# Kernel optimization log

Hardware: AMD Instinct MI355X
Metric: run time of the kernel (lower is better)

Reference implementation:

```python
import jax, jax.numpy as jnp
import numpy as np

S_MIN, S_MAX, ALPHA = 1, 5, 5.0
EPS = 1e-6


def _conv2d_same(x, k):
    # x: [B,1,H,W], k: [1,1,3,3], stride 1, padding 1
    return jax.lax.conv_general_dilated(x, k, (1, 1), ((1, 1), (1, 1)),
                                        dimension_numbers=('NCHW', 'OIHW', 'NCHW'))


def sobel_complexity(x):
    # compute_spatial_complexity_sobel: per-image min-max normalized gradient magnitude
    xg = x.mean(1, keepdims=True)  # [B,1,H,W]
    sx = jnp.array([[1, 0, -1], [2, 0, -2], [1, 0, -1]], x.dtype).reshape(1, 1, 3, 3)
    sy = jnp.array([[1, 2, 1], [0, 0, 0], [-1, -2, -1]], x.dtype).reshape(1, 1, 3, 3)
    gx = _conv2d_same(xg, sx)
    gy = _conv2d_same(xg, sy)
    mag = jnp.sqrt(gx ** 2 + gy ** 2 + EPS)
    mn = mag.min((2, 3), keepdims=True)
    mx = mag.max((2, 3), keepdims=True)
    rng = mx - mn
    c = jnp.where(rng > 0, (mag - mn) / (rng + EPS), jnp.zeros_like(mag))
    return c[:, 0]  # [B,H,W]


def adaptive_steps(m):
    # adaptive_step_from_complexity, fully vectorized
    B, H, W = m.shape
    avg = jnp.ones((1, 1, 3, 3), m.dtype) / 9.0
    lc = _conv2d_same(m[:, None], avg)[:, 0]  # [B,H,W] local complexity
    hm, wm = H // 2, W // 2
    rc = jnp.stack([m[:, :hm, :wm].mean((1, 2)), m[:, :hm, wm:].mean((1, 2)),
                    m[:, hm:, :wm].mean((1, 2)), m[:, hm:, wm:].mean((1, 2))], axis=1)  # [B,4]
    base = S_MAX - jax.nn.sigmoid(ALPHA * (rc - 0.5)) * (S_MAX - S_MIN)
    base = jnp.round(jnp.clip(base, S_MIN, S_MAX)).astype(jnp.int32)  # [B,4]
    adj = jnp.round(jax.nn.sigmoid(ALPHA * (lc - 0.5)) * 2.0 - 1.0).astype(jnp.int32)  # [B,H,W]
    return jnp.clip(base[:, :, None, None] + adj[:, None], S_MIN, S_MAX)  # [B,4,H,W]


def _visits_lr(step):
    # step: [B,R,L] int. Left-to-right adaptive-step traversal along last axis per row.
    # Returns float mask [B,R,L] of visited positions.
    B, R, L = step.shape
    s = jnp.maximum(step, 1)

    def body(j, _):
        valid = j < L                       # [B,R]
        jc = jnp.minimum(j, L - 1)
        st = jnp.take_along_axis(s, jc[:, :, None], -1)[:, :, 0]
        return jnp.where(valid, j + st, j), (jc, valid)

    _, (jcs, valids) = jax.lax.scan(body, jnp.zeros((B, R), jnp.int32), None, length=L)
    jcs = jnp.moveaxis(jcs, 0, -1)          # [B,R,L]
    valids = jnp.moveaxis(valids, 0, -1)    # [B,R,L]
    bi = jnp.arange(B)[:, None, None]
    ri = jnp.arange(R)[None, :, None]
    vis = jnp.zeros((B, R, L), jnp.float32).at[bi, ri, jcs].add(valids.astype(jnp.float32))
    return (vis > 0).astype(jnp.float32)


def _visits_rl(step):
    # Right-to-left traversal == left-to-right on the mirrored step map, mirrored back.
    return jnp.flip(_visits_lr(jnp.flip(step, -1)), -1)


def _forward(x):
    m = sobel_complexity(x)                 # [B,H,W]
    steps = adaptive_steps(m)               # [B,4,H,W]
    v0 = _visits_lr(steps[:, 0])            # rows, left->right
    v1 = _visits_rl(steps[:, 1])            # rows, right->left
    v2 = jnp.swapaxes(_visits_lr(jnp.swapaxes(steps[:, 2], 1, 2)), 1, 2)  # cols, top->down
    v3 = jnp.swapaxes(_visits_rl(jnp.swapaxes(steps[:, 3], 1, 2)), 1, 2)  # cols, bottom->up
    V = v0 + v1 + v2 + v3                   # [B,H,W] visit counts
    # DirectionalScan followed by DirectionalMerge: output = sum_d x*visit_d / (V + 1e-6)
    return x * (V / (V + 1e-6))[:, None]


def setup_inputs() -> dict:
    key = jax.random.key(0)
    x = jax.random.normal(key, (8, 96, 256, 256), dtype=jnp.float32)
    return {"x": x}


def reference(x):
    return _forward(x)
```

## Files before the change

kernel.cpp:

```cpp
#include <hip/hip_runtime.h>
#include <math.h>

#define BB 8
#define CC 96
#define HH 256
#define WW 256
#define HW (HH*WW)

typedef unsigned long long u64;
typedef float f32x4 __attribute__((ext_vector_type(4)));

__global__ void k_mean(const float* __restrict__ x, float* __restrict__ m,
                       unsigned* __restrict__ mn_u, unsigned* __restrict__ mx_u) {
    if (blockIdx.x == 0 && threadIdx.x < 2 * BB) {
        if (threadIdx.x < BB) mn_u[threadIdx.x] = 0x7f800000u;
        else                  mx_u[threadIdx.x - BB] = 0u;
    }
    int blk = blockIdx.x;
    int b = blk >> 8, tile = blk & 255;
    int wv = threadIdx.x >> 6, ln = threadIdx.x & 63;
    int hw4 = tile * 64 + ln;
    const int per = HW / 4;
    const float4* xb = reinterpret_cast<const float4*>(x)
                     + ((size_t)b * CC + wv * 24) * per + hw4;
    double a0 = 0, a1 = 0, a2 = 0, a3 = 0;
#pragma unroll
    for (int c = 0; c < 24; ++c) {
        float4 v = xb[(size_t)c * per];
        a0 += (double)v.x; a1 += (double)v.y; a2 += (double)v.z; a3 += (double)v.w;
    }
    __shared__ double sbuf[4][4][64];
    sbuf[wv][0][ln] = a0; sbuf[wv][1][ln] = a1;
    sbuf[wv][2][ln] = a2; sbuf[wv][3][ln] = a3;
    __syncthreads();
    if (wv == 0) {
        double r0 = sbuf[0][0][ln] + sbuf[1][0][ln] + sbuf[2][0][ln] + sbuf[3][0][ln];
        double r1 = sbuf[0][1][ln] + sbuf[1][1][ln] + sbuf[2][1][ln] + sbuf[3][1][ln];
        double r2 = sbuf[0][2][ln] + sbuf[1][2][ln] + sbuf[2][2][ln] + sbuf[3][2][ln];
        double r3 = sbuf[0][3][ln] + sbuf[1][3][ln] + sbuf[2][3][ln] + sbuf[3][3][ln];
        float4 o;
        o.x = (float)(r0 / 96.0); o.y = (float)(r1 / 96.0);
        o.z = (float)(r2 / 96.0); o.w = (float)(r3 / 96.0);
        reinterpret_cast<float4*>(m)[(size_t)b * per + hw4] = o;
    }
}

__global__ void k_sobel(const float* __restrict__ m, float* __restrict__ mag,
                        unsigned* mn_u, unsigned* mx_u) {
    int row = blockIdx.x;
    int b = row >> 8, h = row & 255, w = threadIdx.x;
    const float* mb = m + (size_t)b * HW;
    auto at = [&](int hh, int ww) -> float {
        if (hh < 0 || hh >= HH || ww < 0 || ww >= WW) return 0.0f;
        return mb[hh * WW + ww];
    };
    float a00 = at(h - 1, w - 1), a01 = at(h - 1, w), a02 = at(h - 1, w + 1);
    float a10 = at(h, w - 1),                         a12 = at(h, w + 1);
    float a20 = at(h + 1, w - 1), a21 = at(h + 1, w), a22 = at(h + 1, w + 1);
    float gx = a00 - a02 + 2.0f * a10 - 2.0f * a12 + a20 - a22;
    float gy = a00 + 2.0f * a01 + a02 - a20 - 2.0f * a21 - a22;
    float mg = sqrtf(gx * gx + gy * gy + 1e-6f);
    mag[row * WW + w] = mg;

    float lmn = mg, lmx = mg;
    for (int off = 32; off; off >>= 1) {
        lmn = fminf(lmn, __shfl_down(lmn, off));
        lmx = fmaxf(lmx, __shfl_down(lmx, off));
    }
    __shared__ float smn[4], smx[4];
    int wv = threadIdx.x >> 6, ln = threadIdx.x & 63;
    if (ln == 0) { smn[wv] = lmn; smx[wv] = lmx; }
    __syncthreads();
    if (threadIdx.x == 0) {
        float bmn = fminf(fminf(smn[0], smn[1]), fminf(smn[2], smn[3]));
        float bmx = fmaxf(fmaxf(smx[0], smx[1]), fmaxf(smx[2], smx[3]));
        atomicMin(&mn_u[b], __float_as_uint(bmn));
        atomicMax(&mx_u[b], __float_as_uint(bmx));
    }
}

__global__ void k_adjpart(const float* __restrict__ mag, const unsigned* __restrict__ mn_u,
                          const unsigned* __restrict__ mx_u, signed char* __restrict__ adj,
                          float* __restrict__ part) {
    int row = blockIdx.x;
    int b = row >> 8, h = row & 255, w = threadIdx.x;
    float mn = __uint_as_float(mn_u[b]);
    float mx = __uint_as_float(mx_u[b]);
    float rng = mx - mn;
    const float* gb = mag + (size_t)b * HW;
    auto cat = [&](int hh, int ww) -> float {
        if (hh < 0 || hh >= HH || ww < 0 || ww >= WW) return 0.0f;
        float mg = gb[hh * WW + ww];
        return (rng > 0.0f) ? (mg - mn) / (rng + 1e-6f) : 0.0f;
    };
    float cc = cat(h, w);

    float r = cc;
    for (int off = 32; off; off >>= 1) r += __shfl_down(r, off);
    __shared__ float s[4];
    int wv = threadIdx.x >> 6, ln = threadIdx.x & 63;
    if (ln == 0) s[wv] = r;
    __syncthreads();
    if (threadIdx.x == 0) {
        part[row * 2 + 0] = s[0] + s[1];
        part[row * 2 + 1] = s[2] + s[3];
    }

    const float w9 = 1.0f / 9.0f;
    float acc = 0.0f;
    acc = fmaf(cat(h - 1, w - 1), w9, acc);
    acc = fmaf(cat(h - 1, w    ), w9, acc);
    acc = fmaf(cat(h - 1, w + 1), w9, acc);
    acc = fmaf(cat(h    , w - 1), w9, acc);
    acc = fmaf(cc,               w9, acc);
    acc = fmaf(cat(h    , w + 1), w9, acc);
    acc = fmaf(cat(h + 1, w - 1), w9, acc);
    acc = fmaf(cat(h + 1, w    ), w9, acc);
    acc = fmaf(cat(h + 1, w + 1), w9, acc);
    float sg = 1.0f / (1.0f + expf(-5.0f * (acc - 0.5f)));
    adj[row * WW + w] = (signed char)(int)rintf(sg * 2.0f - 1.0f);
}

#define SETBIT(j) do { int _j = (j); \
    if (_j < 64) m0 |= 1ull << _j; \
    else if (_j < 128) m1 |= 1ull << (_j - 64); \
    else if (_j < 192) m2 |= 1ull << (_j - 128); \
    else m3 |= 1ull << (_j - 192); } while (0)

__global__ void k_travbase(const signed char* __restrict__ adj, const float* __restrict__ part,
                           u64* __restrict__ masks) {
    int blk = blockIdx.x;
    int dir = blk >> 3, b = blk & 7;
    int t = threadIdx.x;

    __shared__ double sd[128];
    __shared__ int sbs;
    int hlo = (dir >> 1) ? 128 : 0;
    int col = dir & 1;
    if (t < 128) sd[t] = (double)part[((b << 8) + hlo + t) * 2 + col];
    __syncthreads();
    for (int str = 64; str > 0; str >>= 1) {
        if (t < str) sd[t] += sd[t + str];
        __syncthreads();
    }
    if (t == 0) {
        float rc = (float)(sd[0] / 16384.0);
        float sig = 1.0f / (1.0f + expf(-5.0f * (rc - 0.5f)));
        float bsf = 5.0f - sig * 4.0f;
        bsf = fminf(fmaxf(bsf, 1.0f), 5.0f);
        sbs = (int)rintf(bsf);
    }
    __syncthreads();
    int bs = sbs;

    int r = t;
    const signed char* ab = adj + (size_t)b * HW;
    u64 m0 = 0, m1 = 0, m2 = 0, m3 = 0;
    if (dir == 0) {
        int j = 0;
        while (j < WW) {
            SETBIT(j);
            int st = bs + (int)ab[r * WW + j];
            st = st < 1 ? 1 : (st > 5 ? 5 : st);
            j += st;
        }
    } else if (dir == 1) {
        int j = WW - 1;
        while (j >= 0) {
            SETBIT(j);
            int st = bs + (int)ab[r * WW + j];
            st = st < 1 ? 1 : (st > 5 ? 5 : st);
            j -= st;
        }
    } else if (dir == 2) {
        int j = 0;
        while (j < HH) {
            SETBIT(j);
            int st = bs + (int)ab[j * WW + r];
            st = st < 1 ? 1 : (st > 5 ? 5 : st);
            j += st;
        }
    } else {
        int j = HH - 1;
        while (j >= 0) {
            SETBIT(j);
            int st = bs + (int)ab[j * WW + r];
            st = st < 1 ? 1 : (st > 5 ? 5 : st);
            j -= st;
        }
    }
    u64* o = masks + ((size_t)dir * BB * 256 + (b << 8) + r) * 4;
    o[0] = m0; o[1] = m1; o[2] = m2; o[3] = m3;
}

__global__ void k_scale(const u64* __restrict__ masks, float* __restrict__ scale) {
    int row = blockIdx.x;
    int b = row >> 8, h = row & 255, w = threadIdx.x;
    const u64* m0 = masks + (((size_t)0 * BB + b) * 256 + h) * 4;
    const u64* m1 = masks + (((size_t)1 * BB + b) * 256 + h) * 4;
    const u64* m2 = masks + (((size_t)2 * BB + b) * 256 + w) * 4;
    const u64* m3 = masks + (((size_t)3 * BB + b) * 256 + w) * 4;
    int v = (int)((m0[w >> 6] >> (w & 63)) & 1ull)
          + (int)((m1[w >> 6] >> (w & 63)) & 1ull)
          + (int)((m2[h >> 6] >> (h & 63)) & 1ull)
          + (int)((m3[h >> 6] >> (h & 63)) & 1ull);
    float fV = (float)v;
    scale[row * WW + w] = fV / (fV + 1e-6f);
}

__global__ void k_out(const float* __restrict__ x, const float* __restrict__ scale,
                      float* __restrict__ out) {
    const int per_img4 = CC * HW / 4;
    const int hw4n = HW / 4;
    int i = blockIdx.x * blockDim.x + threadIdx.x;
    int b = i / per_img4;
    int hw4 = i & (hw4n - 1);
    f32x4 sv = reinterpret_cast<const f32x4*>(scale)[b * hw4n + hw4];
    f32x4 xv = reinterpret_cast<const f32x4*>(x)[i];
    f32x4 ov = xv * sv;
    __builtin_nontemporal_store(ov, reinterpret_cast<f32x4*>(out) + i);
}

extern "C" void kernel_launch(void* const* d_in, const int* in_sizes, int n_in,
                              void* d_out, int out_size, void* d_ws, size_t ws_size,
                              hipStream_t stream) {
    const float* x = (const float*)d_in[0];
    float* out = (float*)d_out;
    char* ws = (char*)d_ws;

    float* m     = (float*)(ws);
    float* mag   = (float*)(ws + (size_t)2 * 1024 * 1024);
    float* scale = (float*)(ws + (size_t)4 * 1024 * 1024);
    signed char* adj = (signed char*)(ws + (size_t)6 * 1024 * 1024);
    u64* masks   = (u64*)(ws + (size_t)6 * 1024 * 1024 + 524288);
    float* part  = (float*)(ws + (size_t)6 * 1024 * 1024 + 524288 + 262144);
    unsigned* mn_u = (unsigned*)(ws + (size_t)6 * 1024 * 1024 + 524288 + 262144 + 16384);
    unsigned* mx_u = mn_u + 8;

    k_mean<<<BB * 256, 256, 0, stream>>>(x, m, mn_u, mx_u);
    k_sobel<<<BB * HH, 256, 0, stream>>>(m, mag, mn_u, mx_u);
    k_adjpart<<<BB * HH, 256, 0, stream>>>(mag, mn_u, mx_u, adj, part);
    k_travbase<<<32, 256, 0, stream>>>(adj, part, masks);
    k_scale<<<BB * HH, 256, 0, stream>>>(masks, scale);
    k_out<<<(BB * CC * HW / 4) / 256, 256, 0, stream>>>(x, scale, out);
}
```

Measured before the change: 169.0 us.

## Fuse sobel, stencil, traversal and scale into one per-image kernel

Replaces four separate middle kernels with a single 1024-thread kernel per image. The per-image min/max comes from a block-level reduction, so the global atomics are gone, and the adj map and traversal masks now live in LDS instead of global memory. This is meant to cut launch overhead and global round-trips between the stages. In exchange the middle phase runs on only 8 blocks, each looping serially over 64K pixels several times, so latency and low parallelism may dominate.

```diff
diff --git a/kernel.cpp b/kernel.cpp
--- a/kernel.cpp
+++ b/kernel.cpp
@@ -10,12 +10,7 @@
 typedef unsigned long long u64;
 typedef float f32x4 __attribute__((ext_vector_type(4)));
 
-__global__ void k_mean(const float* __restrict__ x, float* __restrict__ m,
-                       unsigned* __restrict__ mn_u, unsigned* __restrict__ mx_u) {
-    if (blockIdx.x == 0 && threadIdx.x < 2 * BB) {
-        if (threadIdx.x < BB) mn_u[threadIdx.x] = 0x7f800000u;
-        else                  mx_u[threadIdx.x - BB] = 0u;
-    }
+__global__ void k_mean(const float* __restrict__ x, float* __restrict__ m) {
     int blk = blockIdx.x;
     int b = blk >> 8, tile = blk & 255;
     int wv = threadIdx.x >> 6, ln = threadIdx.x & 63;
@@ -45,167 +40,160 @@
     }
 }
 
-__global__ void k_sobel(const float* __restrict__ m, float* __restrict__ mag,
-                        unsigned* mn_u, unsigned* mx_u) {
-    int row = blockIdx.x;
-    int b = row >> 8, h = row & 255, w = threadIdx.x;
+#define SETBIT(j) do { int _j = (j); \
+    if (_j < 64) m0 |= 1ull << _j; \
+    else if (_j < 128) m1 |= 1ull << (_j - 64); \
+    else if (_j < 192) m2 |= 1ull << (_j - 128); \
+    else m3 |= 1ull << (_j - 192); } while (0)
+
+__global__ __launch_bounds__(1024)
+void k_middle(const float* __restrict__ m, float* __restrict__ mag,
+              float* __restrict__ scale) {
+    __shared__ signed char adj_s[HW];
+    __shared__ u64 mask_s[1024][4];
+    __shared__ float part_s[256][2];
+    __shared__ float partial_s[256][4];
+    __shared__ double sd[4][128];
+    __shared__ float red_mn[16], red_mx[16];
+    __shared__ float smn_f, smx_f;
+    __shared__ int sbs[4];
+
+    int b = blockIdx.x, tid = threadIdx.x;
     const float* mb = m + (size_t)b * HW;
+    float* gb = mag + (size_t)b * HW;
+    int wv = tid >> 6, ln = tid & 63;
+
     auto at = [&](int hh, int ww) -> float {
         if (hh < 0 || hh >= HH || ww < 0 || ww >= WW) return 0.0f;
         return mb[hh * WW + ww];
     };
-    float a00 = at(h - 1, w - 1), a01 = at(h - 1, w), a02 = at(h - 1, w + 1);
-    float a10 = at(h, w - 1),                         a12 = at(h, w + 1);
-    float a20 = at(h + 1, w - 1), a21 = at(h + 1, w), a22 = at(h + 1, w + 1);
-    float gx = a00 - a02 + 2.0f * a10 - 2.0f * a12 + a20 - a22;
-    float gy = a00 + 2.0f * a01 + a02 - a20 - 2.0f * a21 - a22;
-    float mg = sqrtf(gx * gx + gy * gy + 1e-6f);
-    mag[row * WW + w] = mg;
-
-    float lmn = mg, lmx = mg;
+
+    float lmn = __builtin_inff(), lmx = -__builtin_inff();
+    for (int p = 0; p < 64; ++p) {
+        int idx = p * 1024 + tid;
+        int h = idx >> 8, w = idx & 255;
+        float a00 = at(h - 1, w - 1), a01 = at(h - 1, w), a02 = at(h - 1, w + 1);
+        float a10 = at(h, w - 1),                         a12 = at(h, w + 1);
+        float a20 = at(h + 1, w - 1), a21 = at(h + 1, w), a22 = at(h + 1, w + 1);
+        float gx = a00 - a02 + 2.0f * a10 - 2.0f * a12 + a20 - a22;
+        float gy = a00 + 2.0f * a01 + a02 - a20 - 2.0f * a21 - a22;
+        float mg = sqrtf(gx * gx + gy * gy + 1e-6f);
+        gb[idx] = mg;
+        lmn = fminf(lmn, mg); lmx = fmaxf(lmx, mg);
+    }
     for (int off = 32; off; off >>= 1) {
         lmn = fminf(lmn, __shfl_down(lmn, off));
         lmx = fmaxf(lmx, __shfl_down(lmx, off));
     }
-    __shared__ float smn[4], smx[4];
-    int wv = threadIdx.x >> 6, ln = threadIdx.x & 63;
-    if (ln == 0) { smn[wv] = lmn; smx[wv] = lmx; }
-    __syncthreads();
-    if (threadIdx.x == 0) {
-        float bmn = fminf(fminf(smn[0], smn[1]), fminf(smn[2], smn[3]));
-        float bmx = fmaxf(fmaxf(smx[0], smx[1]), fmaxf(smx[2], smx[3]));
-        atomicMin(&mn_u[b], __float_as_uint(bmn));
-        atomicMax(&mx_u[b], __float_as_uint(bmx));
-    }
-}
-
-__global__ void k_adjpart(const float* __restrict__ mag, const unsigned* __restrict__ mn_u,
-                          const unsigned* __restrict__ mx_u, signed char* __restrict__ adj,
-                          float* __restrict__ part) {
-    int row = blockIdx.x;
-    int b = row >> 8, h = row & 255, w = threadIdx.x;
-    float mn = __uint_as_float(mn_u[b]);
-    float mx = __uint_as_float(mx_u[b]);
-    float rng = mx - mn;
-    const float* gb = mag + (size_t)b * HW;
+    if (ln == 0) { red_mn[wv] = lmn; red_mx[wv] = lmx; }
+    __syncthreads();
+    if (tid == 0) {
+        float a = red_mn[0], c2 = red_mx[0];
+        for (int i = 1; i < 16; ++i) { a = fminf(a, red_mn[i]); c2 = fmaxf(c2, red_mx[i]); }
+        smn_f = a; smx_f = c2;
+    }
+    __syncthreads();
+    float mn = smn_f, mx = smx_f, rng = mx - mn;
     auto cat = [&](int hh, int ww) -> float {
         if (hh < 0 || hh >= HH || ww < 0 || ww >= WW) return 0.0f;
         float mg = gb[hh * WW + ww];
         return (rng > 0.0f) ? (mg - mn) / (rng + 1e-6f) : 0.0f;
     };
-    float cc = cat(h, w);
-
-    float r = cc;
-    for (int off = 32; off; off >>= 1) r += __shfl_down(r, off);
-    __shared__ float s[4];
-    int wv = threadIdx.x >> 6, ln = threadIdx.x & 63;
-    if (ln == 0) s[wv] = r;
-    __syncthreads();
-    if (threadIdx.x == 0) {
-        part[row * 2 + 0] = s[0] + s[1];
-        part[row * 2 + 1] = s[2] + s[3];
-    }
-
+
+    int g = tid >> 8, w2 = tid & 255;
     const float w9 = 1.0f / 9.0f;
-    float acc = 0.0f;
-    acc = fmaf(cat(h - 1, w - 1), w9, acc);
-    acc = fmaf(cat(h - 1, w    ), w9, acc);
-    acc = fmaf(cat(h - 1, w + 1), w9, acc);
-    acc = fmaf(cat(h    , w - 1), w9, acc);
-    acc = fmaf(cc,               w9, acc);
-    acc = fmaf(cat(h    , w + 1), w9, acc);
-    acc = fmaf(cat(h + 1, w - 1), w9, acc);
-    acc = fmaf(cat(h + 1, w    ), w9, acc);
-    acc = fmaf(cat(h + 1, w + 1), w9, acc);
-    float sg = 1.0f / (1.0f + expf(-5.0f * (acc - 0.5f)));
-    adj[row * WW + w] = (signed char)(int)rintf(sg * 2.0f - 1.0f);
-}
-
-#define SETBIT(j) do { int _j = (j); \
-    if (_j < 64) m0 |= 1ull << _j; \
-    else if (_j < 128) m1 |= 1ull << (_j - 64); \
-    else if (_j < 192) m2 |= 1ull << (_j - 128); \
-    else m3 |= 1ull << (_j - 192); } while (0)
-
-__global__ void k_travbase(const signed char* __restrict__ adj, const float* __restrict__ part,
-                           u64* __restrict__ masks) {
-    int blk = blockIdx.x;
-    int dir = blk >> 3, b = blk & 7;
-    int t = threadIdx.x;
-
-    __shared__ double sd[128];
-    __shared__ int sbs;
-    int hlo = (dir >> 1) ? 128 : 0;
-    int col = dir & 1;
-    if (t < 128) sd[t] = (double)part[((b << 8) + hlo + t) * 2 + col];
+    for (int p = 0; p < 64; ++p) {
+        int h = p * 4 + g;
+        float cc = cat(h, w2);
+        float r = cc;
+        for (int off = 32; off; off >>= 1) r += __shfl_down(r, off);
+        if (ln == 0) partial_s[h][w2 >> 6] = r;
+        float acc = 0.0f;
+        acc = fmaf(cat(h - 1, w2 - 1), w9, acc);
+        acc = fmaf(cat(h - 1, w2    ), w9, acc);
+        acc = fmaf(cat(h - 1, w2 + 1), w9, acc);
+        acc = fmaf(cat(h    , w2 - 1), w9, acc);
+        acc = fmaf(cc,                w9, acc);
+        acc = fmaf(cat(h    , w2 + 1), w9, acc);
+        acc = fmaf(cat(h + 1, w2 - 1), w9, acc);
+        acc = fmaf(cat(h + 1, w2    ), w9, acc);
+        acc = fmaf(cat(h + 1, w2 + 1), w9, acc);
+        float sg = 1.0f / (1.0f + expf(-5.0f * (acc - 0.5f)));
+        adj_s[h * 256 + w2] = (signed char)(int)rintf(sg * 2.0f - 1.0f);
+    }
+    __syncthreads();
+    if (tid < 512) {
+        int row = tid >> 1, col = tid & 1;
+        part_s[row][col] = partial_s[row][2 * col] + partial_s[row][2 * col + 1];
+    }
+    __syncthreads();
+
+    if (tid < 512) {
+        int d = tid >> 7, t = tid & 127;
+        int hlo = (d >> 1) ? 128 : 0, col = d & 1;
+        sd[d][t] = (double)part_s[hlo + t][col];
+    }
     __syncthreads();
     for (int str = 64; str > 0; str >>= 1) {
-        if (t < str) sd[t] += sd[t + str];
+        if (tid < 512) {
+            int d = tid >> 7, t = tid & 127;
+            if (t < str) sd[d][t] += sd[d][t + str];
+        }
         __syncthreads();
     }
-    if (t == 0) {
-        float rc = (float)(sd[0] / 16384.0);
+    if (tid < 4) {
+        float rc = (float)(sd[tid][0] / 16384.0);
         float sig = 1.0f / (1.0f + expf(-5.0f * (rc - 0.5f)));
         float bsf = 5.0f - sig * 4.0f;
         bsf = fminf(fmaxf(bsf, 1.0f), 5.0f);
-        sbs = (int)rintf(bsf);
-    }
-    __syncthreads();
-    int bs = sbs;
-
-    int r = t;
-    const signed char* ab = adj + (size_t)b * HW;
-    u64 m0 = 0, m1 = 0, m2 = 0, m3 = 0;
-    if (dir == 0) {
-        int j = 0;
-        while (j < WW) {
-            SETBIT(j);
-            int st = bs + (int)ab[r * WW + j];
-            st = st < 1 ? 1 : (st > 5 ? 5 : st);
-            j += st;
+        sbs[tid] = (int)rintf(bsf);
+    }
+    __syncthreads();
+
+    {
+        int dir = tid >> 8, rr = tid & 255;
+        int bs = sbs[dir];
+        u64 m0 = 0, m1 = 0, m2 = 0, m3 = 0;
+        if (dir == 0) {
+            int j = 0;
+            while (j < WW) { SETBIT(j);
+                int st = bs + (int)adj_s[rr * 256 + j];
+                st = st < 1 ? 1 : (st > 5 ? 5 : st); j += st; }
+        } else if (dir == 1) {
+            int j = WW - 1;
+            while (j >= 0) { SETBIT(j);
+                int st = bs + (int)adj_s[rr * 256 + j];
+                st = st < 1 ? 1 : (st > 5 ? 5 : st); j -= st; }
+        } else if (dir == 2) {
+            int j = 0;
+            while (j < HH) { SETBIT(j);
+                int st = bs + (int)adj_s[j * 256 + rr];
+                st = st < 1 ? 1 : (st > 5 ? 5 : st); j += st; }
+        } else {
+            int j = HH - 1;
+            while (j >= 0) { SETBIT(j);
+                int st = bs + (int)adj_s[j * 256 + rr];
+                st = st < 1 ? 1 : (st > 5 ? 5 : st); j -= st; }
         }
-    } else if (dir == 1) {
-        int j = WW - 1;
-        while (j >= 0) {
-            SETBIT(j);
-            int st = bs + (int)ab[r * WW + j];
-            st = st < 1 ? 1 : (st > 5 ? 5 : st);
-            j -= st;
-        }
-    } else if (dir == 2) {
-        int j = 0;
-        while (j < HH) {
-            SETBIT(j);
-            int st = bs + (int)ab[j * WW + r];
-            st = st < 1 ? 1 : (st > 5 ? 5 : st);
-            j += st;
-        }
-    } else {
-        int j = HH - 1;
-        while (j >= 0) {
-            SETBIT(j);
-            int st = bs + (int)ab[j * WW + r];
-            st = st < 1 ? 1 : (st > 5 ? 5 : st);
-            j -= st;
-        }
-    }
-    u64* o = masks + ((size_t)dir * BB * 256 + (b << 8) + r) * 4;
-    o[0] = m0; o[1] = m1; o[2] = m2; o[3] = m3;
-}
-
-__global__ void k_scale(const u64* __restrict__ masks, float* __restrict__ scale) {
-    int row = blockIdx.x;
-    int b = row >> 8, h = row & 255, w = threadIdx.x;
-    const u64* m0 = masks + (((size_t)0 * BB + b) * 256 + h) * 4;
-    const u64* m1 = masks + (((size_t)1 * BB + b) * 256 + h) * 4;
-    const u64* m2 = masks + (((size_t)2 * BB + b) * 256 + w) * 4;
-    const u64* m3 = masks + (((size_t)3 * BB + b) * 256 + w) * 4;
-    int v = (int)((m0[w >> 6] >> (w & 63)) & 1ull)
-          + (int)((m1[w >> 6] >> (w & 63)) & 1ull)
-          + (int)((m2[h >> 6] >> (h & 63)) & 1ull)
-          + (int)((m3[h >> 6] >> (h & 63)) & 1ull);
-    float fV = (float)v;
-    scale[row * WW + w] = fV / (fV + 1e-6f);
+        mask_s[tid][0] = m0; mask_s[tid][1] = m1;
+        mask_s[tid][2] = m2; mask_s[tid][3] = m3;
+    }
+    __syncthreads();
+
+    for (int p = 0; p < 64; ++p) {
+        int idx = p * 1024 + tid;
+        int h = idx >> 8, w = idx & 255;
+        const u64* q0 = mask_s[0 * 256 + h];
+        const u64* q1 = mask_s[1 * 256 + h];
+        const u64* q2 = mask_s[2 * 256 + w];
+        const u64* q3 = mask_s[3 * 256 + w];
+        int v = (int)((q0[w >> 6] >> (w & 63)) & 1ull)
+              + (int)((q1[w >> 6] >> (w & 63)) & 1ull)
+              + (int)((q2[h >> 6] >> (h & 63)) & 1ull)
+              + (int)((q3[h >> 6] >> (h & 63)) & 1ull);
+        float fV = (float)v;
+        scale[(size_t)b * HW + idx] = fV / (fV + 1e-6f);
+    }
 }
 
 __global__ void k_out(const float* __restrict__ x, const float* __restrict__ scale,
@@ -231,16 +219,8 @@
     float* m     = (float*)(ws);
     float* mag   = (float*)(ws + (size_t)2 * 1024 * 1024);
     float* scale = (float*)(ws + (size_t)4 * 1024 * 1024);
-    signed char* adj = (signed char*)(ws + (size_t)6 * 1024 * 1024);
-    u64* masks   = (u64*)(ws + (size_t)6 * 1024 * 1024 + 524288);
-    float* part  = (float*)(ws + (size_t)6 * 1024 * 1024 + 524288 + 262144);
-    unsigned* mn_u = (unsigned*)(ws + (size_t)6 * 1024 * 1024 + 524288 + 262144 + 16384);
-    unsigned* mx_u = mn_u + 8;
-
-    k_mean<<<BB * 256, 256, 0, stream>>>(x, m, mn_u, mx_u);
-    k_sobel<<<BB * HH, 256, 0, stream>>>(m, mag, mn_u, mx_u);
-    k_adjpart<<<BB * HH, 256, 0, stream>>>(mag, mn_u, mx_u, adj, part);
-    k_travbase<<<32, 256, 0, stream>>>(adj, part, masks);
-    k_scale<<<BB * HH, 256, 0, stream>>>(masks, scale);
+
+    k_mean<<<BB * 256, 256, 0, stream>>>(x, m);
+    k_middle<<<BB, 1024, 0, stream>>>(m, mag, scale);
     k_out<<<(BB * CC * HW / 4) / 256, 256, 0, stream>>>(x, scale, out);
 }
```

New measurement: 340.6 us. 2.02x slower.
